# Kernel tuning notes

Hardware: AMD Instinct MI355X
Metric: run time of the kernel (lower is better)

## Reference

```python
import jax, jax.numpy as jnp
import numpy as np

N_NODES = 100000
N_EDGES = 1600000
D_IN = 64
D_HID = 64
D_OUT = 64
TOPK = 32


def _num_params(din, dout):
    return din * dout + dout


def setup_inputs() -> dict:
    key = jax.random.key(0)
    ks = jax.random.split(key, 16)
    x = jax.random.normal(ks[0], (N_NODES, D_IN), dtype=jnp.float32)
    edge_index = jax.random.randint(ks[1], (2, N_EDGES), 0, N_NODES, dtype=jnp.int64)
    # GCN layer params (PyG GCNConv: lin.weight [out,in], bias [out])
    w0 = jax.random.normal(ks[2], (D_HID, D_IN), dtype=jnp.float32) * (1.0 / np.sqrt(D_IN))
    b0 = jnp.zeros((D_HID,), dtype=jnp.float32)
    w1 = jax.random.normal(ks[3], (D_OUT, D_HID), dtype=jnp.float32) * (1.0 / np.sqrt(D_HID))
    b1 = jnp.zeros((D_OUT,), dtype=jnp.float32)
    # summarization vectors p (torch.randn init)
    p0 = jax.random.normal(ks[4], (D_IN,), dtype=jnp.float32)
    p1 = jax.random.normal(ks[5], (D_HID,), dtype=jnp.float32)
    # GRU cells: hidden = num_params, input = topk * feature_dim
    np0 = _num_params(D_IN, D_HID)
    np1 = _num_params(D_HID, D_OUT)
    gi0 = TOPK * D_IN
    gi1 = TOPK * D_HID
    s0 = 1.0 / np.sqrt(np0)
    s1 = 1.0 / np.sqrt(np1)
    wih0 = jax.random.uniform(ks[6], (3 * np0, gi0), jnp.float32, -s0, s0)
    whh0 = jax.random.uniform(ks[7], (3 * np0, np0), jnp.float32, -s0, s0)
    bih0 = jax.random.uniform(ks[8], (3 * np0,), jnp.float32, -s0, s0)
    bhh0 = jax.random.uniform(ks[9], (3 * np0,), jnp.float32, -s0, s0)
    wih1 = jax.random.uniform(ks[10], (3 * np1, gi1), jnp.float32, -s1, s1)
    whh1 = jax.random.uniform(ks[11], (3 * np1, np1), jnp.float32, -s1, s1)
    bih1 = jax.random.uniform(ks[12], (3 * np1,), jnp.float32, -s1, s1)
    bhh1 = jax.random.uniform(ks[13], (3 * np1,), jnp.float32, -s1, s1)
    return {"x": x, "edge_index": edge_index,
            "p0": p0, "p1": p1,
            "w0": w0, "b0": b0, "w1": w1, "b1": b1,
            "wih0": wih0, "whh0": whh0, "bih0": bih0, "bhh0": bhh0,
            "wih1": wih1, "whh1": whh1, "bih1": bih1, "bhh1": bhh1}


def _summarize(h, p, k):
    # attention summary: top-k nodes by h @ p_norm, weighted by tanh(score)
    p_norm = p / (jnp.linalg.norm(p) + 1e-8)
    y = h @ p_norm                      # [N]
    _, idx = jax.lax.top_k(y, k)        # k <= N here, matches torch.topk branch
    w = jnp.tanh(y)
    return h[idx] * w[idx][:, None]     # [k, feat]


def _gru_cell(xv, hv, wih, whh, bih, bhh):
    gi = xv @ wih.T + bih
    gh = hv @ whh.T + bhh
    ir, iz, inew = jnp.split(gi, 3)
    hr, hz, hnew = jnp.split(gh, 3)
    r = jax.nn.sigmoid(ir + hr)
    z = jax.nn.sigmoid(iz + hz)
    n = jnp.tanh(inew + r * hnew)
    return (1.0 - z) * n + z * hv


def _gcn_conv(h, src, dst, weight, bias, n_nodes):
    # PyG GCNConv: x' = x @ W.T; add self-loops; sym-norm aggregation; + bias
    xw = h @ weight.T
    loop = jnp.arange(n_nodes, dtype=src.dtype)
    s = jnp.concatenate([src, loop])
    d = jnp.concatenate([dst, loop])
    deg = jax.ops.segment_sum(jnp.ones(s.shape[0], dtype=xw.dtype), d,
                              num_segments=n_nodes)
    dinv = jnp.where(deg > 0, jax.lax.rsqrt(jnp.maximum(deg, 1e-12)), 0.0)
    norm = dinv[s] * dinv[d]
    msgs = xw[s] * norm[:, None]
    out = jax.ops.segment_sum(msgs, d, num_segments=n_nodes)
    return out + bias


def reference(x, edge_index, p0, p1, w0, b0, w1, b1,
              wih0, whh0, bih0, bhh0, wih1, whh1, bih1, bhh1):
    src, dst = edge_index[0], edge_index[1]
    n = x.shape[0]
    h = x
    layers = [
        (p0, w0, b0, wih0, whh0, bih0, bhh0, D_IN, D_HID, True),
        (p1, w1, b1, wih1, whh1, bih1, bhh1, D_HID, D_OUT, False),
    ]
    for (p, w, b, wih, whh, bih, bhh, din, dout, relu) in layers:
        # summarize node embeddings -> GRU input (Z_t.T.flatten(): feature-major)
        Z = _summarize(h, p, TOPK)                  # [TOPK, din]
        z_flat = Z.T.reshape(-1)                    # [din*TOPK]
        # initial GRU hidden = flattened current GCN params (weight then bias)
        h0 = jnp.concatenate([w.reshape(-1), b])    # [din*dout + dout]
        new_w = _gru_cell(z_flat, h0, wih, whh, bih, bhh)
        weight = new_w[: din * dout].reshape(dout, din)
        bias = new_w[din * dout:]
        h = _gcn_conv(h, src, dst, weight, bias, n)
        if relu:
            h = jax.nn.relu(h)  # dropout is identity in eval mode
    return h
```

## Files before the change

### kernel.cpp

```cpp
#include <hip/hip_runtime.h>
#include <math.h>

#define N_NODES 100000
#define N_EDGES 1600000
#define D 64
#define NP 4160
#define GI3 12480
#define GIN 2048
#define TOPK 32
#define MV_BLKS 3120

#define NB 391
#define SCAT_ITEMS 4096
#define SCAT_BLKS 391
#define COLCAP 6144

#define OFF_PN     0u
#define OFF_MISC   64u
#define OFF_IDX    80u
#define OFF_WSEL   112u
#define OFF_ZFLAT  144u
#define OFF_NEWW   2192u
#define OFF_GI     6400u
#define OFF_GH     18880u
#define OFF_HIST   31360u
#define OFF_Y      96896u
#define OFF_DEG    196896u
#define OFF_DINV   296896u
#define OFF_ROWPTR 396896u
#define OFF_CURSOR 496898u
#define OFF_COL    596898u
#define OFF_CAND   2196898u
#define OFF_XW     2396898u
#define OFF_H1     8796898u
#define OFF_BSUM   15196898u
#define WS_FLOATS  15197026u

__device__ __forceinline__ unsigned fkey(float f) {
    unsigned u = __float_as_uint(f);
    return u ^ ((u & 0x80000000u) ? 0xFFFFFFFFu : 0x80000000u);
}

__global__ void k_zero32(unsigned* __restrict__ p, int n) {
    int i = blockIdx.x * blockDim.x + threadIdx.x;
    if (i < n) p[i] = 0u;
}

__global__ void k_bcount(const int* __restrict__ dst, unsigned* __restrict__ bcnt, int ne) {
    __shared__ unsigned h[NB];
    int t = threadIdx.x;
    for (int i = t; i < NB; i += 256) h[i] = 0u;
    __syncthreads();
    int base0 = blockIdx.x * SCAT_ITEMS;
    #pragma unroll
    for (int k = 0; k < 16; ++k) {
        int i = base0 + k * 256 + t;
        if (i < ne) atomicAdd(&h[dst[i] >> 8], 1u);
    }
    __syncthreads();
    for (int i = t; i < NB; i += 256) if (h[i]) atomicAdd(&bcnt[i], h[i]);
}

__global__ void k_bscan(const unsigned* __restrict__ bcnt, unsigned* __restrict__ bbase,
                        unsigned* __restrict__ bcur, unsigned* __restrict__ rowptr) {
    __shared__ unsigned sc[512];
    int t = threadIdx.x;
    unsigned v = (t < NB) ? bcnt[t] : 0u;
    sc[t] = v; __syncthreads();
    for (int off = 1; off < 512; off <<= 1) {
        unsigned a = (t >= off) ? sc[t - off] : 0u;
        __syncthreads();
        sc[t] += a;
        __syncthreads();
    }
    unsigned ex = sc[t] - v;
    if (t <= NB) bbase[t] = ex;
    if (t < NB) bcur[t] = ex;
    if (t == 511) rowptr[N_NODES] = sc[511];
}

__global__ void k_bscatter(const int* __restrict__ src, const int* __restrict__ dst,
                           unsigned* __restrict__ bcur, unsigned* __restrict__ ebuf, int ne) {
    __shared__ unsigned hist[NB];
    __shared__ unsigned sc[512];
    __shared__ unsigned basel[NB];
    __shared__ unsigned lcur[NB];
    __shared__ unsigned gdst[NB];
    __shared__ unsigned sbuf[SCAT_ITEMS];
    __shared__ unsigned short sb[SCAT_ITEMS];
    int t = threadIdx.x;
    for (int i = t; i < NB; i += 256) hist[i] = 0u;
    __syncthreads();
    int base0 = blockIdx.x * SCAT_ITEMS;
    unsigned key[16]; int bk[16];
    #pragma unroll
    for (int k = 0; k < 16; ++k) {
        int i = base0 + k * 256 + t;
        if (i < ne) {
            int d = dst[i];
            bk[k] = d >> 8;
            key[k] = ((unsigned)(d & 255) << 24) | (unsigned)src[i];
            atomicAdd(&hist[bk[k]], 1u);
        } else bk[k] = -1;
    }
    __syncthreads();
    {
        unsigned v0 = hist[t];
        unsigned v1 = (t + 256 < NB) ? hist[t + 256] : 0u;
        sc[t] = v0; sc[t + 256] = v1; __syncthreads();
        for (int off = 1; off < 512; off <<= 1) {
            unsigned a0 = (t >= off) ? sc[t - off] : 0u;
            unsigned a1 = (t + 256 >= off) ? sc[t + 256 - off] : 0u;
            __syncthreads();
            sc[t] += a0; sc[t + 256] += a1;
            __syncthreads();
        }
    }
    for (int i = t; i < NB; i += 256) {
        unsigned b0 = sc[i] - hist[i];
        basel[i] = b0; lcur[i] = b0;
    }
    __syncthreads();
    for (int i = t; i < NB; i += 256) if (hist[i]) gdst[i] = atomicAdd(&bcur[i], hist[i]);
    #pragma unroll
    for (int k = 0; k < 16; ++k) if (bk[k] >= 0) {
        unsigned p = atomicAdd(&lcur[bk[k]], 1u);
        sbuf[p] = key[k]; sb[p] = (unsigned short)bk[k];
    }
    __syncthreads();
    int cnt = min(SCAT_ITEMS, ne - base0);
    for (int j = t; j < cnt; j += 256) {
        unsigned b = sb[j];
        ebuf[gdst[b] + ((unsigned)j - basel[b])] = sbuf[j];
    }
}

__global__ void k_bcsr(const unsigned* __restrict__ ebuf, const unsigned* __restrict__ bbase,
                       unsigned* __restrict__ rowptr, float* __restrict__ dinv,
                       int* __restrict__ col, int n) {
    __shared__ unsigned deg[256];
    __shared__ unsigned sc[256];
    __shared__ unsigned lcur[256];
    __shared__ int colbuf[COLCAP];
    int b = blockIdx.x, t = threadIdx.x;
    int lo = b << 8;
    unsigned e0 = bbase[b], e1 = bbase[b + 1];
    deg[t] = 0u; __syncthreads();
    for (unsigned j = e0 + t; j < e1; j += 256) atomicAdd(&deg[ebuf[j] >> 24], 1u);
    __syncthreads();
    sc[t] = deg[t]; __syncthreads();
    for (int off = 1; off < 256; off <<= 1) {
        unsigned a = (t >= off) ? sc[t - off] : 0u;
        __syncthreads();
        sc[t] += a;
        __syncthreads();
    }
    unsigned lrp = sc[t] - deg[t];
    if (lo + t < n) {
        rowptr[lo + t] = e0 + lrp;
        dinv[lo + t] = rsqrtf((float)(deg[t] + 1u));
    }
    lcur[t] = lrp; __syncthreads();
    for (unsigned j = e0 + t; j < e1; j += 256) {
        unsigned k = ebuf[j];
        unsigned p = atomicAdd(&lcur[k >> 24], 1u);
        if (p < COLCAP) colbuf[p] = (int)(k & 0xFFFFFFu);
        else col[e0 + p] = (int)(k & 0xFFFFFFu);
    }
    __syncthreads();
    unsigned cnt = e1 - e0;
    for (unsigned j = t; j < cnt && j < COLCAP; j += 256) col[e0 + j] = colbuf[j];
}

__global__ void k_pnorm_zh(const float* __restrict__ p, float* __restrict__ pn,
                           unsigned* __restrict__ misc, unsigned* __restrict__ hist) {
    int g = blockIdx.x * blockDim.x + threadIdx.x;
    hist[g] = 0u;
    if (blockIdx.x == 0) {
        int t = threadIdx.x;
        if (t < 64) {
            float v = p[t];
            float s = v * v;
            for (int o = 32; o; o >>= 1) s += __shfl_down(s, o, 64);
            s = __shfl(s, 0, 64);
            pn[t] = v / (sqrtf(s) + 1e-8f);
        }
        if (t < 16) misc[t] = 0u;
    }
}

__global__ void k_y_hist(const float* __restrict__ h, const float* __restrict__ pn,
                         float* __restrict__ y, unsigned* __restrict__ hist, int n) {
    int wave = (blockIdx.x * blockDim.x + threadIdx.x) >> 6;
    int lane = threadIdx.x & 63;
    int nw = (gridDim.x * blockDim.x) >> 6;
    float p = pn[lane];
    for (int i = wave; i < n; i += 4 * nw) {
        int i1 = i + nw, i2 = i + 2 * nw, i3 = i + 3 * nw;
        float v0 = h[(size_t)i * D + lane] * p;
        float v1 = (i1 < n) ? h[(size_t)i1 * D + lane] * p : 0.f;
        float v2 = (i2 < n) ? h[(size_t)i2 * D + lane] * p : 0.f;
        float v3 = (i3 < n) ? h[(size_t)i3 * D + lane] * p : 0.f;
        #pragma unroll
        for (int o = 32; o; o >>= 1) {
            v0 += __shfl_down(v0, o, 64);
            v1 += __shfl_down(v1, o, 64);
            v2 += __shfl_down(v2, o, 64);
            v3 += __shfl_down(v3, o, 64);
        }
        if (lane == 0) {
            y[i] = v0; atomicAdd(&hist[fkey(v0) >> 16], 1u);
            if (i1 < n) { y[i1] = v1; atomicAdd(&hist[fkey(v1) >> 16], 1u); }
            if (i2 < n) { y[i2] = v2; atomicAdd(&hist[fkey(v2) >> 16], 1u); }
            if (i3 < n) { y[i3] = v3; atomicAdd(&hist[fkey(v3) >> 16], 1u); }
        }
    }
}

__global__ void k_thresh(const unsigned* __restrict__ hist, unsigned* __restrict__ misc) {
    __shared__ unsigned cs[256];
    __shared__ unsigned s2[256];
    __shared__ int tstar;
    int t = threadIdx.x;
    unsigned sum = 0;
    for (int j = 0; j < 256; ++j) sum += hist[t * 256 + j];
    cs[t] = sum; __syncthreads();
    for (int off = 1; off < 256; off <<= 1) {
        unsigned add = (t + off < 256) ? cs[t + off] : 0u;
        __syncthreads();
        cs[t] += add;
        __syncthreads();
    }
    if (cs[t] >= TOPK && (t == 255 || cs[t + 1] < TOPK)) tstar = t;
    __syncthreads();
    int ts = tstar;
    unsigned above = (ts == 255) ? 0u : cs[ts + 1];
    s2[t] = hist[ts * 256 + t]; __syncthreads();
    for (int off = 1; off < 256; off <<= 1) {
        unsigned add = (t + off < 256) ? s2[t + off] : 0u;
        __syncthreads();
        s2[t] += add;
        __syncthreads();
    }
    if (above + s2[t] >= TOPK && (t == 255 || above + s2[t + 1] < TOPK))
        misc[1] = (unsigned)(ts * 256 + t);
}

__global__ void k_compact(const float* __restrict__ y, unsigned* __restrict__ misc,
                          unsigned long long* __restrict__ cand, int n) {
    int i = blockIdx.x * blockDim.x + threadIdx.x;
    if (i >= n) return;
    unsigned thr = misc[1];
    unsigned k = fkey(y[i]);
    if ((k >> 16) >= thr) {
        unsigned pos = atomicAdd(&misc[0], 1u);
        cand[pos] = ((unsigned long long)k << 32) | (unsigned)(0xFFFFFFFFu - (unsigned)i);
    }
}

__global__ void k_select(const float* __restrict__ y, const unsigned* __restrict__ misc,
                         unsigned long long* __restrict__ cand,
                         int* __restrict__ idxb, float* __restrict__ wsel) {
    int t = threadIdx.x;
    int C = (int)misc[0];
    for (int k = 0; k < TOPK; ++k) {
        unsigned long long m = 0ull;
        for (int j = t; j < C; j += 64) { unsigned long long c = cand[j]; if (c > m) m = c; }
        for (int o = 32; o; o >>= 1) {
            unsigned long long other = __shfl_down(m, o, 64);
            if (other > m) m = other;
        }
        unsigned long long best = __shfl(m, 0, 64);
        for (int j = t; j < C; j += 64) if (cand[j] == best) cand[j] = 0ull;
        if (t == 0) {
            int idx = (int)(0xFFFFFFFFu - (unsigned)(best & 0xFFFFFFFFull));
            idxb[k] = idx;
            wsel[k] = tanhf(y[idx]);
        }
    }
}

__global__ void k_zflat(const float* __restrict__ h, const int* __restrict__ idxb,
                        const float* __restrict__ wsel, float* __restrict__ z) {
    int t = blockIdx.x * blockDim.x + threadIdx.x;
    if (t < GIN) {
        int k = t & 31, d = t >> 5;
        z[t] = h[(size_t)idxb[k] * D + d] * wsel[k];
    }
}

__global__ void k_mv2(const float* __restrict__ W0, const float* __restrict__ bia0,
                      const float* __restrict__ vA0, int lenA0, const float* __restrict__ vB0,
                      float* __restrict__ out0, int cols0,
                      const float* __restrict__ W1, const float* __restrict__ bia1,
                      const float* __restrict__ vA1, int lenA1, const float* __restrict__ vB1,
                      float* __restrict__ out1, int cols1) {
    extern __shared__ float v[];
    int seg = (blockIdx.x >= MV_BLKS);
    const float* W    = seg ? W1   : W0;
    const float* bias = seg ? bia1 : bia0;
    const float* vA   = seg ? vA1  : vA0;
    const float* vB   = seg ? vB1  : vB0;
    float* out        = seg ? out1 : out0;
    int lenA          = seg ? lenA1 : lenA0;
    int cols          = seg ? cols1 : cols0;
    int lb = blockIdx.x - (seg ? MV_BLKS : 0);
    for (int j = threadIdx.x; j < cols; j += blockDim.x)
        v[j] = (j < lenA) ? vA[j] : vB[j - lenA];
    __syncthreads();
    int row = ((lb * blockDim.x + threadIdx.x) >> 6);
    int lane = threadIdx.x & 63;
    if (row >= GI3) return;
    const float4* Wr = (const float4*)(W + (size_t)row * cols);
    int n4 = cols >> 2;
    float acc = 0.f;
    for (int j = lane; j < n4; j += 64) {
        float4 w4 = Wr[j];
        acc += w4.x * v[4 * j] + w4.y * v[4 * j + 1] + w4.z * v[4 * j + 2] + w4.w * v[4 * j + 3];
    }
    for (int o = 32; o; o >>= 1) acc += __shfl_down(acc, o, 64);
    if (lane == 0) out[row] = acc + bias[row];
}

__global__ void k_gru(const float* __restrict__ gi, const float* __restrict__ gh,
                      const float* __restrict__ w, const float* __restrict__ b,
                      float* __restrict__ neww) {
    int j = blockIdx.x * blockDim.x + threadIdx.x;
    if (j >= NP) return;
    float r = 1.f / (1.f + expf(-(gi[j] + gh[j])));
    float z = 1.f / (1.f + expf(-(gi[NP + j] + gh[NP + j])));
    float n = tanhf(gi[2 * NP + j] + r * gh[2 * NP + j]);
    float h0 = (j < 4096) ? w[j] : b[j - 4096];
    neww[j] = (1.f - z) * n + z * h0;
}

__global__ void k_xw(const float* __restrict__ h, const float* __restrict__ neww,
                     const float* __restrict__ dinv, float* __restrict__ sxw, int n) {
    __shared__ float WT[64 * 64];
    for (int t = threadIdx.x; t < 4096; t += blockDim.x) {
        int o = t >> 6, d = t & 63;
        WT[d * 64 + o] = neww[t];
    }
    __syncthreads();
    int wave = (blockIdx.x * blockDim.x + threadIdx.x) >> 6;
    int lane = threadIdx.x & 63;
    int nw = (gridDim.x * blockDim.x) >> 6;
    for (int i = wave; i < n; i += nw) {
        float hv = h[(size_t)i * D + lane];
        float acc = 0.f;
        #pragma unroll 16
        for (int d = 0; d < 64; ++d) {
            float hd = __shfl(hv, d, 64);
            acc += hd * WT[d * 64 + lane];
        }
        sxw[(size_t)i * D + lane] = dinv[i] * acc;
    }
}

__global__ void k_agg(const float* __restrict__ sxw, const float* __restrict__ dinv,
                      const unsigned* __restrict__ rowptr, const int* __restrict__ col,
                      const float* __restrict__ neww, float* __restrict__ out,
                      int n, int relu) {
    int wave = (blockIdx.x * blockDim.x + threadIdx.x) >> 6;
    int lane = threadIdx.x & 63;
    int nw = (gridDim.x * blockDim.x) >> 6;
    float bias = neww[4096 + lane];
    for (int v = wave; v < n; v += nw) {
        unsigned p0 = rowptr[v], p1 = rowptr[v + 1];
        float dv = dinv[v];
        float acc = sxw[(size_t)v * D + lane];
        for (unsigned base = p0; base < p1; base += 64) {
            int cnt = (int)min(64u, p1 - base);
            int s = 0;
            if (lane < cnt) s = col[base + lane];
            for (int j = 0; j < cnt; ++j) {
                int sj = __shfl(s, j, 64);
                acc += sxw[(size_t)sj * D + lane];
            }
        }
        float r = bias + dv * acc;
        if (relu) r = fmaxf(r, 0.f);
        out[(size_t)v * D + lane] = r;
    }
}

extern "C" void kernel_launch(void* const* d_in, const int* in_sizes, int n_in,
                              void* d_out, int out_size, void* d_ws, size_t ws_size,
                              hipStream_t stream) {
    if (ws_size < (size_t)WS_FLOATS * 4) return;

    const float* x = (const float*)d_in[0];
    const int* src = (const int*)d_in[1];
    const int* dst = src + N_EDGES;
    const float* P[2]   = {(const float*)d_in[2],  (const float*)d_in[3]};
    const float* W[2]   = {(const float*)d_in[4],  (const float*)d_in[6]};
    const float* B[2]   = {(const float*)d_in[5],  (const float*)d_in[7]};
    const float* WIH[2] = {(const float*)d_in[8],  (const float*)d_in[12]};
    const float* WHH[2] = {(const float*)d_in[9],  (const float*)d_in[13]};
    const float* BIH[2] = {(const float*)d_in[10], (const float*)d_in[14]};
    const float* BHH[2] = {(const float*)d_in[11], (const float*)d_in[15]};

    float* ws = (float*)d_ws;
    float* pn = ws + OFF_PN;
    unsigned* misc = (unsigned*)(ws + OFF_MISC);
    int* idxb = (int*)(ws + OFF_IDX);
    float* wsel = ws + OFF_WSEL;
    float* zflat = ws + OFF_ZFLAT;
    float* neww = ws + OFF_NEWW;
    float* gi = ws + OFF_GI;
    float* gh = ws + OFF_GH;
    unsigned* hist = (unsigned*)(ws + OFF_HIST);
    float* y = ws + OFF_Y;
    unsigned* bcnt  = (unsigned*)(ws + OFF_DEG);
    unsigned* bbase = (unsigned*)(ws + OFF_DEG) + 512;
    unsigned* bcur  = (unsigned*)(ws + OFF_DEG) + 1024;
    float* dinv = ws + OFF_DINV;
    unsigned* rowptr = (unsigned*)(ws + OFF_ROWPTR);
    int* col = (int*)(ws + OFF_COL);
    unsigned long long* cand = (unsigned long long*)(ws + OFF_CAND);
    float* xw = ws + OFF_XW;
    unsigned* ebuf = (unsigned*)(ws + OFF_XW);
    float* h1 = ws + OFF_H1;
    float* out = (float*)d_out;

    hipLaunchKernelGGL(k_zero32, dim3((NB + 255) / 256), dim3(256), 0, stream, bcnt, NB);
    hipLaunchKernelGGL(k_bcount, dim3(SCAT_BLKS), dim3(256), 0, stream, dst, bcnt, N_EDGES);
    hipLaunchKernelGGL(k_bscan, dim3(1), dim3(512), 0, stream, bcnt, bbase, bcur, rowptr);
    hipLaunchKernelGGL(k_bscatter, dim3(SCAT_BLKS), dim3(256), 0, stream, src, dst, bcur, ebuf, N_EDGES);
    hipLaunchKernelGGL(k_bcsr, dim3(NB), dim3(256), 0, stream, ebuf, bbase, rowptr, dinv, col, N_NODES);

    for (int l = 0; l < 2; ++l) {
        const float* h = (l == 0) ? x : h1;
        float* ho = (l == 0) ? h1 : out;
        hipLaunchKernelGGL(k_pnorm_zh, dim3(256), dim3(256), 0, stream, P[l], pn, misc, hist);
        hipLaunchKernelGGL(k_y_hist, dim3(1024), dim3(256), 0, stream, h, pn, y, hist, N_NODES);
        hipLaunchKernelGGL(k_thresh, dim3(1), dim3(256), 0, stream, hist, misc);
        hipLaunchKernelGGL(k_compact, dim3((N_NODES + 255) / 256), dim3(256), 0, stream, y, misc, cand, N_NODES);
        hipLaunchKernelGGL(k_select, dim3(1), dim3(64), 0, stream, y, misc, cand, idxb, wsel);
        hipLaunchKernelGGL(k_zflat, dim3(8), dim3(256), 0, stream, h, idxb, wsel, zflat);
        hipLaunchKernelGGL(k_mv2, dim3(2 * MV_BLKS), dim3(256), NP * 4, stream,
                           WIH[l], BIH[l], zflat, GIN, zflat, gi, GIN,
                           WHH[l], BHH[l], W[l], 4096, B[l], gh, NP);
        hipLaunchKernelGGL(k_gru, dim3((NP + 255) / 256), dim3(256), 0, stream, gi, gh, W[l], B[l], neww);
        hipLaunchKernelGGL(k_xw, dim3(2048), dim3(256), 0, stream, h, neww, dinv, xw, N_NODES);
        hipLaunchKernelGGL(k_agg, dim3(4096), dim3(256), 0, stream, xw, dinv, rowptr, col, neww, ho,
                           N_NODES, (l == 0) ? 1 : 0);
    }
}
```

Measured before the change: 1.362 ms.

## Fuse top-k threshold, compaction, selection and gather into one kernel; unroll aggregation

```diff
diff --git a/kernel.cpp b/kernel.cpp
--- a/kernel.cpp
+++ b/kernel.cpp
@@ -9,6 +9,7 @@
 #define GIN 2048
 #define TOPK 32
 #define MV_BLKS 3120
+#define TCAP 2048
 
 #define NB 391
 #define SCAT_ITEMS 4096
@@ -217,75 +218,100 @@
     }
 }
 
-__global__ void k_thresh(const unsigned* __restrict__ hist, unsigned* __restrict__ misc) {
-    __shared__ unsigned cs[256];
-    __shared__ unsigned s2[256];
-    __shared__ int tstar;
+__global__ void k_topsel(const unsigned* __restrict__ hist, const float* __restrict__ y,
+                         unsigned long long* __restrict__ cand, const float* __restrict__ h,
+                         float* __restrict__ z, int n) {
+    __shared__ unsigned s64[1024];
+    __shared__ unsigned long long scand[TCAP];
+    __shared__ unsigned long long smax[1024];
+    __shared__ unsigned scount;
+    __shared__ unsigned sthr;
+    __shared__ int sg;
+    __shared__ int sidx[TOPK];
+    __shared__ float swv[TOPK];
     int t = threadIdx.x;
-    unsigned sum = 0;
-    for (int j = 0; j < 256; ++j) sum += hist[t * 256 + j];
-    cs[t] = sum; __syncthreads();
-    for (int off = 1; off < 256; off <<= 1) {
-        unsigned add = (t + off < 256) ? cs[t + off] : 0u;
-        __syncthreads();
-        cs[t] += add;
-        __syncthreads();
-    }
-    if (cs[t] >= TOPK && (t == 255 || cs[t + 1] < TOPK)) tstar = t;
-    __syncthreads();
-    int ts = tstar;
-    unsigned above = (ts == 255) ? 0u : cs[ts + 1];
-    s2[t] = hist[ts * 256 + t]; __syncthreads();
-    for (int off = 1; off < 256; off <<= 1) {
-        unsigned add = (t + off < 256) ? s2[t + off] : 0u;
-        __syncthreads();
-        s2[t] += add;
-        __syncthreads();
-    }
-    if (above + s2[t] >= TOPK && (t == 255 || above + s2[t + 1] < TOPK))
-        misc[1] = (unsigned)(ts * 256 + t);
-}
-
-__global__ void k_compact(const float* __restrict__ y, unsigned* __restrict__ misc,
-                          unsigned long long* __restrict__ cand, int n) {
-    int i = blockIdx.x * blockDim.x + threadIdx.x;
-    if (i >= n) return;
-    unsigned thr = misc[1];
-    unsigned k = fkey(y[i]);
-    if ((k >> 16) >= thr) {
-        unsigned pos = atomicAdd(&misc[0], 1u);
-        cand[pos] = ((unsigned long long)k << 32) | (unsigned)(0xFFFFFFFFu - (unsigned)i);
-    }
-}
-
-__global__ void k_select(const float* __restrict__ y, const unsigned* __restrict__ misc,
-                         unsigned long long* __restrict__ cand,
-                         int* __restrict__ idxb, float* __restrict__ wsel) {
-    int t = threadIdx.x;
-    int C = (int)misc[0];
-    for (int k = 0; k < TOPK; ++k) {
-        unsigned long long m = 0ull;
-        for (int j = t; j < C; j += 64) { unsigned long long c = cand[j]; if (c > m) m = c; }
-        for (int o = 32; o; o >>= 1) {
-            unsigned long long other = __shfl_down(m, o, 64);
-            if (other > m) m = other;
-        }
-        unsigned long long best = __shfl(m, 0, 64);
-        for (int j = t; j < C; j += 64) if (cand[j] == best) cand[j] = 0ull;
-        if (t == 0) {
-            int idx = (int)(0xFFFFFFFFu - (unsigned)(best & 0xFFFFFFFFull));
-            idxb[k] = idx;
-            wsel[k] = tanhf(y[idx]);
-        }
-    }
-}
-
-__global__ void k_zflat(const float* __restrict__ h, const int* __restrict__ idxb,
-                        const float* __restrict__ wsel, float* __restrict__ z) {
-    int t = blockIdx.x * blockDim.x + threadIdx.x;
-    if (t < GIN) {
-        int k = t & 31, d = t >> 5;
-        z[t] = h[(size_t)idxb[k] * D + d] * wsel[k];
+    unsigned gs = 0;
+    #pragma unroll 8
+    for (int j = 0; j < 64; ++j) gs += hist[t * 64 + j];
+    s64[t] = gs; __syncthreads();
+    for (int off = 1; off < 1024; off <<= 1) {
+        unsigned add = (t + off < 1024) ? s64[t + off] : 0u;
+        __syncthreads();
+        s64[t] += add;
+        __syncthreads();
+    }
+    if (s64[t] >= TOPK && (t == 1023 || s64[t + 1] < TOPK)) sg = t;
+    __syncthreads();
+    if (t == 0) {
+        int g = sg;
+        unsigned run = (g == 1023) ? 0u : s64[g + 1];
+        unsigned thr = (unsigned)(g * 64);
+        for (int i = 63; i >= 0; --i) {
+            run += hist[g * 64 + i];
+            if (run >= TOPK) { thr = (unsigned)(g * 64 + i); break; }
+        }
+        sthr = thr; scount = 0;
+    }
+    __syncthreads();
+    unsigned thr = sthr;
+    for (int i = t; i < n; i += 1024) {
+        unsigned k = fkey(y[i]);
+        if ((k >> 16) >= thr) {
+            unsigned pos = atomicAdd(&scount, 1u);
+            unsigned long long pk = ((unsigned long long)k << 32) | (unsigned)(0xFFFFFFFFu - (unsigned)i);
+            if (pos < TCAP) scand[pos] = pk; else cand[pos] = pk;
+        }
+    }
+    __syncthreads();
+    int C = (int)scount;
+    if (C <= 64) {
+        if (t < 64) {
+            unsigned long long mine = (t < C) ? scand[t] : 0ull;
+            for (int k = 0; k < TOPK; ++k) {
+                unsigned long long m = mine;
+                for (int o = 32; o; o >>= 1) {
+                    unsigned long long other = __shfl_down(m, o, 64);
+                    if (other > m) m = other;
+                }
+                unsigned long long best = __shfl(m, 0, 64);
+                if (mine == best) mine = 0ull;
+                if (t == 0) {
+                    int idx = (int)(0xFFFFFFFFu - (unsigned)(best & 0xFFFFFFFFull));
+                    sidx[k] = idx;
+                    swv[k] = tanhf(y[idx]);
+                }
+            }
+        }
+        __syncthreads();
+    } else {
+        for (int k = 0; k < TOPK; ++k) {
+            unsigned long long m = 0ull;
+            for (int j = t; j < C; j += 1024) {
+                unsigned long long c = (j < TCAP) ? scand[j] : cand[j];
+                if (c > m) m = c;
+            }
+            smax[t] = m; __syncthreads();
+            for (int off = 512; off; off >>= 1) {
+                if (t < off) { if (smax[t + off] > smax[t]) smax[t] = smax[t + off]; }
+                __syncthreads();
+            }
+            unsigned long long best = smax[0];
+            __syncthreads();
+            for (int j = t; j < C; j += 1024) {
+                if (j < TCAP) { if (scand[j] == best) scand[j] = 0ull; }
+                else if (cand[j] == best) cand[j] = 0ull;
+            }
+            if (t == 0) {
+                int idx = (int)(0xFFFFFFFFu - (unsigned)(best & 0xFFFFFFFFull));
+                sidx[k] = idx;
+                swv[k] = tanhf(y[idx]);
+            }
+            __syncthreads();
+        }
+    }
+    for (int e = t; e < GIN; e += 1024) {
+        int k = e & 31, d = e >> 5;
+        z[e] = h[(size_t)sidx[k] * D + d] * swv[k];
     }
 }
 
@@ -369,16 +395,36 @@
         unsigned p0 = rowptr[v], p1 = rowptr[v + 1];
         float dv = dinv[v];
         float acc = sxw[(size_t)v * D + lane];
+        float acc1 = 0.f;
         for (unsigned base = p0; base < p1; base += 64) {
             int cnt = (int)min(64u, p1 - base);
             int s = 0;
             if (lane < cnt) s = col[base + lane];
-            for (int j = 0; j < cnt; ++j) {
-                int sj = __shfl(s, j, 64);
-                acc += sxw[(size_t)sj * D + lane];
-            }
-        }
-        float r = bias + dv * acc;
+            int j = 0;
+            for (; j + 8 <= cnt; j += 8) {
+                int s0 = __shfl(s, j, 64);
+                int s1 = __shfl(s, j + 1, 64);
+                int s2 = __shfl(s, j + 2, 64);
+                int s3 = __shfl(s, j + 3, 64);
+                int s4 = __shfl(s, j + 4, 64);
+                int s5 = __shfl(s, j + 5, 64);
+                int s6 = __shfl(s, j + 6, 64);
+                int s7 = __shfl(s, j + 7, 64);
+                float a0 = sxw[(size_t)s0 * D + lane];
+                float a1 = sxw[(size_t)s1 * D + lane];
+                float a2 = sxw[(size_t)s2 * D + lane];
+                float a3 = sxw[(size_t)s3 * D + lane];
+                float a4 = sxw[(size_t)s4 * D + lane];
+                float a5 = sxw[(size_t)s5 * D + lane];
+                float a6 = sxw[(size_t)s6 * D + lane];
+                float a7 = sxw[(size_t)s7 * D + lane];
+                acc  += (a0 + a2) + (a4 + a6);
+                acc1 += (a1 + a3) + (a5 + a7);
+            }
+            for (; j < cnt; ++j)
+                acc += sxw[(size_t)__shfl(s, j, 64) * D + lane];
+        }
+        float r = bias + dv * (acc + acc1);
         if (relu) r = fmaxf(r, 0.f);
         out[(size_t)v * D + lane] = r;
     }
@@ -403,8 +449,6 @@
     float* ws = (float*)d_ws;
     float* pn = ws + OFF_PN;
     unsigned* misc = (unsigned*)(ws + OFF_MISC);
-    int* idxb = (int*)(ws + OFF_IDX);
-    float* wsel = ws + OFF_WSEL;
     float* zflat = ws + OFF_ZFLAT;
     float* neww = ws + OFF_NEWW;
     float* gi = ws + OFF_GI;
@@ -434,10 +478,7 @@
         float* ho = (l == 0) ? h1 : out;
         hipLaunchKernelGGL(k_pnorm_zh, dim3(256), dim3(256), 0, stream, P[l], pn, misc, hist);
         hipLaunchKernelGGL(k_y_hist, dim3(1024), dim3(256), 0, stream, h, pn, y, hist, N_NODES);
-        hipLaunchKernelGGL(k_thresh, dim3(1), dim3(256), 0, stream, hist, misc);
-        hipLaunchKernelGGL(k_compact, dim3((N_NODES + 255) / 256), dim3(256), 0, stream, y, misc, cand, N_NODES);
-        hipLaunchKernelGGL(k_select, dim3(1), dim3(64), 0, stream, y, misc, cand, idxb, wsel);
-        hipLaunchKernelGGL(k_zflat, dim3(8), dim3(256), 0, stream, h, idxb, wsel, zflat);
+        hipLaunchKernelGGL(k_topsel, dim3(1), dim3(1024), 0, stream, hist, y, cand, h, zflat, N_NODES);
         hipLaunchKernelGGL(k_mv2, dim3(2 * MV_BLKS), dim3(256), NP * 4, stream,
                            WIH[l], BIH[l], zflat, GIN, zflat, gi, GIN,
                            WHH[l], BHH[l], W[l], 4096, B[l], gh, NP);
```

New measurement: 1.339 ms. Within noise of the previous version (-1.7%).
